# Kernel tuning notes

Measured on AMD Instinct MI355X. Metric: run time of the kernel, lower is better.

The kernel has to match this reference:

```python
import jax, jax.numpy as jnp
import numpy as np
from jax import lax

VOCAB = 50000
EMB = 10
HID = 16


def setup_inputs() -> dict:
    key = jax.random.key(0)
    ks = jax.random.split(key, 8)
    B, T = 4096, 512
    x = jax.random.randint(ks[0], (B, T), 0, VOCAB + 1)
    emb = jax.random.normal(ks[1], (VOCAB + 1, EMB), dtype=jnp.float32)
    emb = emb.at[0].set(0.0)  # padding_idx=0 row is zeros
    s_ih = 1.0 / np.sqrt(HID)
    Wih = jax.random.uniform(ks[2], (4 * HID, EMB), minval=-s_ih, maxval=s_ih, dtype=jnp.float32)
    Whh = jax.random.uniform(ks[3], (4 * HID, HID), minval=-s_ih, maxval=s_ih, dtype=jnp.float32)
    bih = jax.random.uniform(ks[4], (4 * HID,), minval=-s_ih, maxval=s_ih, dtype=jnp.float32)
    bhh = jax.random.uniform(ks[5], (4 * HID,), minval=-s_ih, maxval=s_ih, dtype=jnp.float32)
    Wfc = jax.random.uniform(ks[6], (1, HID), minval=-s_ih, maxval=s_ih, dtype=jnp.float32)
    bfc = jax.random.uniform(ks[7], (1,), minval=-s_ih, maxval=s_ih, dtype=jnp.float32)
    return {"x": x, "emb": emb, "Wih": Wih, "Whh": Whh, "bih": bih, "bhh": bhh, "Wfc": Wfc, "bfc": bfc}


def _lstm_last_h(xe, Wih, Whh, bih, bhh):
    # xe: [B, T, EMB] -> final hidden state [B, HID]. PyTorch gate order: i, f, g, o.
    B = xe.shape[0]
    h0 = jnp.zeros((B, HID), dtype=xe.dtype)
    c0 = jnp.zeros((B, HID), dtype=xe.dtype)
    # Precompute input projections for all timesteps: [T, B, 4H]
    xproj = jnp.einsum('btе,ge->btg'.replace('\u0435', 'e'), xe, Wih) + bih + bhh
    xproj = xproj.transpose(1, 0, 2)

    def step(carry, xp_t):
        h, c = carry
        gates = xp_t + h @ Whh.T  # [B, 4H]
        i, f, g, o = jnp.split(gates, 4, axis=-1)
        i = jax.nn.sigmoid(i)
        f = jax.nn.sigmoid(f)
        g = jnp.tanh(g)
        o = jax.nn.sigmoid(o)
        c = f * c + i * g
        h = o * jnp.tanh(c)
        return (h, c), None

    (h, _), _ = lax.scan(step, (h0, c0), xproj)
    return h


def reference(x, emb, Wih, Whh, bih, bhh, Wfc, bfc):
    xe = emb[x]  # [B, T, EMB] embedding lookup (padding row 0 is zero)
    h = _lstm_last_h(xe, Wih, Whh, bih, bhh)  # [B, HID]
    out = h @ Wfc.T + bfc  # [B, 1]
    return jax.nn.sigmoid(out)
```

## Files before the change

### kernel.cpp

```cpp
#include <hip/hip_runtime.h>

#define T_LEN 512
#define NHID 16
#define NEMB 10
#define VOCAB1 50001
#define IROW 521

typedef float v2f __attribute__((ext_vector_type(2)));

__global__ __launch_bounds__(256) void build_table(
    const float* __restrict__ emb, const float* __restrict__ Wih,
    const float* __restrict__ bih, const float* __restrict__ bhh,
    float* __restrict__ tbl)
{
    const int tid = blockIdx.x * 256 + threadIdx.x;
    if (tid >= VOCAB1 * 16) return;
    const int v = tid >> 4, j = tid & 15;
    float e[NEMB];
    #pragma unroll
    for (int i = 0; i < NEMB; ++i) e[i] = emb[v * NEMB + i];
    float o[4];
    #pragma unroll
    for (int q = 0; q < 4; ++q) {
        const int r = q * 16 + j;
        float a = bih[r] + bhh[r];
        #pragma unroll
        for (int i = 0; i < NEMB; ++i) a += e[i] * Wih[r * NEMB + i];
        o[q] = a;
    }
    ((float4*)tbl)[tid] = make_float4(o[0], o[1], o[2], o[3]);
}

__global__ __launch_bounds__(256) void lstm_dpk_kernel(
    const int*   __restrict__ x,
    const float* __restrict__ tbl,
    const float* __restrict__ Whh,
    const float* __restrict__ Wfc,
    const float* __restrict__ bfc,
    float*       __restrict__ out)
{
    __shared__ int idxs[16][IROW];

    const int tid = threadIdx.x;
    const int j   = tid & 15;
    const int lb  = tid >> 4;
    const int batch = blockIdx.x * 16 + lb;

    #pragma unroll 1
    for (int b = 0; b < 16; ++b) {
        const int* xr = x + (size_t)(blockIdx.x * 16 + b) * T_LEN;
        for (int t = tid; t < IROW; t += 256)
            idxs[b][t] = (t < T_LEN) ? (xr[t] << 4) : 0;
    }
    __syncthreads();

    v2f wp[4][8];
    #pragma unroll
    for (int q = 0; q < 4; ++q) {
        const int row = (q * 16 + j) * NHID;
        #pragma unroll
        for (int s = 0; s < 8; ++s)
            wp[q][s] = (v2f){Whh[row + ((j - 2 * s) & 15)],
                             Whh[row + ((j - 2 * s - 1) & 15)]};
    }

    float h = 0.f, c = 0.f;
    const float NL2E  = -1.44269504088896f;
    const float NL2E2 = -2.88539008177793f;
    const float4* t4 = (const float4*)tbl;

    float4 pf[4];
    int iv[4];
    #pragma unroll
    for (int s = 0; s < 4; ++s) {
        pf[s] = t4[idxs[lb][s] + j];
        iv[s] = idxs[lb][4 + s];
    }

    #pragma unroll 1
    for (int t = 0; t < T_LEN; t += 4) {
        int ivn[4];
        #pragma unroll
        for (int u = 0; u < 4; ++u) ivn[u] = idxs[lb][t + 8 + u];

        #pragma unroll
        for (int u = 0; u < 4; ++u) {
            const float4 tb = pf[u];
            pf[u] = t4[iv[u] + j];

            const int hvi = __builtin_bit_cast(int, h);
            #define ROR(r) __builtin_bit_cast(float, \
                __builtin_amdgcn_update_dpp(0, hvi, 0x120 + (r), 0xF, 0xF, true))
            v2f hrp[8];
            hrp[0] = (v2f){h,       ROR(1)};
            hrp[1] = (v2f){ROR(2),  ROR(3)};
            hrp[2] = (v2f){ROR(4),  ROR(5)};
            hrp[3] = (v2f){ROR(6),  ROR(7)};
            hrp[4] = (v2f){ROR(8),  ROR(9)};
            hrp[5] = (v2f){ROR(10), ROR(11)};
            hrp[6] = (v2f){ROR(12), ROR(13)};
            hrp[7] = (v2f){ROR(14), ROR(15)};
            #undef ROR

            v2f a0 = (v2f){tb.x, 0.f}, b0 = (v2f){0.f, 0.f};
            v2f a1 = (v2f){tb.y, 0.f}, b1 = (v2f){0.f, 0.f};
            v2f a2 = (v2f){tb.z, 0.f}, b2 = (v2f){0.f, 0.f};
            v2f a3 = (v2f){tb.w, 0.f}, b3 = (v2f){0.f, 0.f};
            #pragma unroll
            for (int s = 0; s < 4; ++s) {
                a0 += hrp[s] * wp[0][s];  b0 += hrp[s + 4] * wp[0][s + 4];
                a1 += hrp[s] * wp[1][s];  b1 += hrp[s + 4] * wp[1][s + 4];
                a2 += hrp[s] * wp[2][s];  b2 += hrp[s + 4] * wp[2][s + 4];
                a3 += hrp[s] * wp[3][s];  b3 += hrp[s + 4] * wp[3][s + 4];
            }
            const v2f s0 = a0 + b0, s1 = a1 + b1, s2 = a2 + b2, s3 = a3 + b3;
            const float v0 = s0.x + s0.y, v1 = s1.x + s1.y;
            const float v2 = s2.x + s2.y, v3 = s3.x + s3.y;

            const float ig = __builtin_amdgcn_rcpf(1.f + __builtin_amdgcn_exp2f(v0 * NL2E));
            const float fg = __builtin_amdgcn_rcpf(1.f + __builtin_amdgcn_exp2f(v1 * NL2E));
            const float gg = 2.f * __builtin_amdgcn_rcpf(1.f + __builtin_amdgcn_exp2f(v2 * NL2E2)) - 1.f;
            const float og = __builtin_amdgcn_rcpf(1.f + __builtin_amdgcn_exp2f(v3 * NL2E));

            c = fg * c + ig * gg;
            const float tc = 2.f * __builtin_amdgcn_rcpf(1.f + __builtin_amdgcn_exp2f(c * NL2E2)) - 1.f;
            h = og * tc;
        }

        #pragma unroll
        for (int u = 0; u < 4; ++u) iv[u] = ivn[u];
    }

    float s = h * Wfc[j];
    s += __shfl_xor(s, 1, 64);
    s += __shfl_xor(s, 2, 64);
    s += __shfl_xor(s, 4, 64);
    s += __shfl_xor(s, 8, 64);
    if (j == 0)
        out[batch] = __builtin_amdgcn_rcpf(1.f + __builtin_amdgcn_exp2f((s + bfc[0]) * NL2E));
}

__global__ __launch_bounds__(256) void lstm_fb_kernel(
    const int*   __restrict__ x,
    const float* __restrict__ emb,
    const float* __restrict__ Wih,
    const float* __restrict__ Whh,
    const float* __restrict__ bih,
    const float* __restrict__ bhh,
    const float* __restrict__ Wfc,
    const float* __restrict__ bfc,
    float*       __restrict__ out)
{
    __shared__ int   idx_lds[T_LEN][17];
    __shared__ float hx[16][20];

    const int tid  = threadIdx.x;
    const int lane = tid & 63;
    const int j    = lane & 15;
    const int lb   = tid >> 4;
    const int batch = blockIdx.x * 16 + lb;

    for (int i = tid; i < 16 * T_LEN; i += 256) {
        const int b = i & 15;
        const int t = i >> 4;
        idx_lds[t][b] = x[(blockIdx.x * 16 + b) * T_LEN + t];
    }

    float wih[4][NEMB], bias[4];
    v2f w[4][8];
    #pragma unroll
    for (int q = 0; q < 4; ++q) {
        const int r = j + 16 * q;
        #pragma unroll
        for (int e = 0; e < NEMB; ++e) wih[q][e] = Wih[r * NEMB + e];
        #pragma unroll
        for (int p = 0; p < 8; ++p)
            w[q][p] = (v2f){Whh[r * NHID + 2 * p], Whh[r * NHID + 2 * p + 1]};
        bias[q] = bih[r] + bhh[r];
    }

    __syncthreads();

    v2f h2[8];
    #pragma unroll
    for (int p = 0; p < 8; ++p) h2[p] = (v2f){0.f, 0.f};
    float c = 0.f;

    const float NL2E  = -1.44269504088896f;
    const float NL2E2 = -2.88539008177793f;
    const float4* hp = (const float4*)&hx[lb][0];

    float2 xa, xb, xc, xd, xe2;
    {
        const float2* er = (const float2*)(emb + (long)idx_lds[0][lb] * NEMB);
        xa = er[0]; xb = er[1]; xc = er[2]; xd = er[3]; xe2 = er[4];
    }
    int idx_n = idx_lds[1][lb];

    #pragma unroll 1
    for (int t = 0; t < T_LEN; ++t) {
        const float xv[NEMB] = {xa.x, xa.y, xb.x, xb.y, xc.x, xc.y,
                                xd.x, xd.y, xe2.x, xe2.y};
        if (t + 1 < T_LEN) {
            const float2* er = (const float2*)(emb + (long)idx_n * NEMB);
            xa = er[0]; xb = er[1]; xc = er[2]; xd = er[3]; xe2 = er[4];
        }
        const int idx_nn = (t + 2 < T_LEN) ? idx_lds[t + 2][lb] : 0;

        float v[4];
        #pragma unroll
        for (int q = 0; q < 4; ++q) {
            float a = bias[q];
            #pragma unroll
            for (int e = 0; e < NEMB; ++e) a += xv[e] * wih[q][e];
            v[q] = a;
        }
        v2f a0 = (v2f){v[0], 0.f}, a1 = (v2f){v[1], 0.f};
        v2f a2 = (v2f){v[2], 0.f}, a3 = (v2f){v[3], 0.f};
        #pragma unroll
        for (int p = 0; p < 8; ++p) {
            a0 += h2[p] * w[0][p];
            a1 += h2[p] * w[1][p];
            a2 += h2[p] * w[2][p];
            a3 += h2[p] * w[3][p];
        }
        const float vi = a0.x + a0.y, vf = a1.x + a1.y;
        const float vg = a2.x + a2.y, vo = a3.x + a3.y;

        const float ig = __builtin_amdgcn_rcpf(1.f + __builtin_amdgcn_exp2f(vi * NL2E));
        const float fg = __builtin_amdgcn_rcpf(1.f + __builtin_amdgcn_exp2f(vf * NL2E));
        const float gg = 2.f * __builtin_amdgcn_rcpf(1.f + __builtin_amdgcn_exp2f(vg * NL2E2)) - 1.f;
        const float og = __builtin_amdgcn_rcpf(1.f + __builtin_amdgcn_exp2f(vo * NL2E));

        c = fg * c + ig * gg;
        const float tc = 2.f * __builtin_amdgcn_rcpf(1.f + __builtin_amdgcn_exp2f(c * NL2E2)) - 1.f;
        const float hv = og * tc;

        hx[lb][j] = hv;
        const float4 b0 = hp[0], b1 = hp[1], b2 = hp[2], b3 = hp[3];
        h2[0] = (v2f){b0.x, b0.y}; h2[1] = (v2f){b0.z, b0.w};
        h2[2] = (v2f){b1.x, b1.y}; h2[3] = (v2f){b1.z, b1.w};
        h2[4] = (v2f){b2.x, b2.y}; h2[5] = (v2f){b2.z, b2.w};
        h2[6] = (v2f){b3.x, b3.y}; h2[7] = (v2f){b3.z, b3.w};

        idx_n = idx_nn;
    }

    if (j == 0) {
        float logit = bfc[0];
        #pragma unroll
        for (int p = 0; p < 8; ++p)
            logit += h2[p].x * Wfc[2 * p] + h2[p].y * Wfc[2 * p + 1];
        out[batch] = __builtin_amdgcn_rcpf(1.f + __builtin_amdgcn_exp2f(logit * NL2E));
    }
}

extern "C" void kernel_launch(void* const* d_in, const int* in_sizes, int n_in,
                              void* d_out, int out_size, void* d_ws, size_t ws_size,
                              hipStream_t stream) {
    const int*   x   = (const int*)  d_in[0];
    const float* emb = (const float*)d_in[1];
    const float* Wih = (const float*)d_in[2];
    const float* Whh = (const float*)d_in[3];
    const float* bih = (const float*)d_in[4];
    const float* bhh = (const float*)d_in[5];
    const float* Wfc = (const float*)d_in[6];
    const float* bfc = (const float*)d_in[7];
    float* outp = (float*)d_out;

    const int B = in_sizes[0] / T_LEN;
    const size_t TABLE_BYTES = (size_t)VOCAB1 * 64 * sizeof(float);

    if (ws_size >= TABLE_BYTES) {
        float* tbl = (float*)d_ws;
        build_table<<<(VOCAB1 * 16 + 255) / 256, 256, 0, stream>>>(emb, Wih, bih, bhh, tbl);
        lstm_dpk_kernel<<<B / 16, 256, 0, stream>>>(x, tbl, Whh, Wfc, bfc, outp);
    } else {
        lstm_fb_kernel<<<B / 16, 256, 0, stream>>>(x, emb, Wih, Whh, bih, bhh, Wfc, bfc, outp);
    }
}
```

Before: 164.0 us.

## Split LSTM gate computation across two lane halves per batch row

Each batch row now uses 32 lanes instead of 16. Each half-group computes two of the four gate pre-activations: lanes with hi=0 compute i and f, and lanes with hi=1 compute g and o. The halves then exchange results with a ds_swizzle. The table layout is changed to match, so each lane fetches a float2 rather than a float4. This halves the per-step serial dot-product and transcendental work on the recurrence critical path, but doubles the thread count, halves the rows per block, and adds cross-lane swizzle latency each step.

```diff
diff --git a/kernel.cpp b/kernel.cpp
--- a/kernel.cpp
+++ b/kernel.cpp
@@ -8,7 +8,7 @@
 
 typedef float v2f __attribute__((ext_vector_type(2)));
 
-__global__ __launch_bounds__(256) void build_table(
+__global__ __launch_bounds__(256) void build_table2(
     const float* __restrict__ emb, const float* __restrict__ Wih,
     const float* __restrict__ bih, const float* __restrict__ bhh,
     float* __restrict__ tbl)
@@ -28,10 +28,15 @@
         for (int i = 0; i < NEMB; ++i) a += e[i] * Wih[r * NEMB + i];
         o[q] = a;
     }
-    ((float4*)tbl)[tid] = make_float4(o[0], o[1], o[2], o[3]);
-}
-
-__global__ __launch_bounds__(256) void lstm_dpk_kernel(
+    float2* t2 = (float2*)tbl;
+    t2[v * 32 + j]      = make_float2(o[0], o[1]);
+    t2[v * 32 + 16 + j] = make_float2(o[2], o[3]);
+}
+
+#define ROR_F(hvi, r) __builtin_bit_cast(float, \
+    __builtin_amdgcn_update_dpp(0, hvi, 0x120 + (r), 0xF, 0xF, true))
+
+__global__ __launch_bounds__(256) void lstm_gs_kernel(
     const int*   __restrict__ x,
     const float* __restrict__ tbl,
     const float* __restrict__ Whh,
@@ -39,41 +44,51 @@
     const float* __restrict__ bfc,
     float*       __restrict__ out)
 {
-    __shared__ int idxs[16][IROW];
+    __shared__ int idxs[8][IROW];
 
     const int tid = threadIdx.x;
-    const int j   = tid & 15;
-    const int lb  = tid >> 4;
-    const int batch = blockIdx.x * 16 + lb;
+    const int l   = tid & 63;
+    const int j   = l & 15;
+    const int hi  = (l >> 4) & 1;
+    const int lb  = tid >> 5;
+    const int batch = blockIdx.x * 8 + lb;
 
     #pragma unroll 1
-    for (int b = 0; b < 16; ++b) {
-        const int* xr = x + (size_t)(blockIdx.x * 16 + b) * T_LEN;
+    for (int b = 0; b < 8; ++b) {
+        const int* xr = x + (size_t)(blockIdx.x * 8 + b) * T_LEN;
         for (int t = tid; t < IROW; t += 256)
-            idxs[b][t] = (t < T_LEN) ? (xr[t] << 4) : 0;
+            idxs[b][t] = (t < T_LEN) ? (xr[t] << 5) : 0;
     }
     __syncthreads();
 
-    v2f wp[4][8];
-    #pragma unroll
-    for (int q = 0; q < 4; ++q) {
-        const int row = (q * 16 + j) * NHID;
-        #pragma unroll
-        for (int s = 0; s < 8; ++s)
-            wp[q][s] = (v2f){Whh[row + ((j - 2 * s) & 15)],
-                             Whh[row + ((j - 2 * s - 1) & 15)]};
-    }
-
-    float h = 0.f, c = 0.f;
+    v2f wpA[8], wpB[8];
+    {
+        const int rA = (2 * hi) * 16 + j;
+        const int rB = rA + 16;
+        #pragma unroll
+        for (int s = 0; s < 8; ++s) {
+            const int k0 = (j - 2 * s) & 15, k1 = (j - 2 * s - 1) & 15;
+            wpA[s] = (v2f){Whh[rA * NHID + k0], Whh[rA * NHID + k1]};
+            wpB[s] = (v2f){Whh[rB * NHID + k0], Whh[rB * NHID + k1]};
+        }
+    }
+
     const float NL2E  = -1.44269504088896f;
     const float NL2E2 = -2.88539008177793f;
-    const float4* t4 = (const float4*)tbl;
-
-    float4 pf[4];
+    const bool  hib = (hi != 0);
+    const float sA = hib ? NL2E2 : NL2E;
+    const float mA = hib ? 2.f : 1.f;
+    const float bA = hib ? -1.f : 0.f;
+
+    float h = 0.f, c = 0.f;
+    const float2* t2 = (const float2*)tbl;
+    const int foff = hi * 16 + j;
+
+    float2 pf[4];
     int iv[4];
     #pragma unroll
     for (int s = 0; s < 4; ++s) {
-        pf[s] = t4[idxs[lb][s] + j];
+        pf[s] = t2[idxs[lb][s] + foff];
         iv[s] = idxs[lb][4 + s];
     }
 
@@ -85,46 +100,47 @@
 
         #pragma unroll
         for (int u = 0; u < 4; ++u) {
-            const float4 tb = pf[u];
-            pf[u] = t4[iv[u] + j];
+            const float2 tb = pf[u];
+            pf[u] = t2[iv[u] + foff];
 
             const int hvi = __builtin_bit_cast(int, h);
-            #define ROR(r) __builtin_bit_cast(float, \
-                __builtin_amdgcn_update_dpp(0, hvi, 0x120 + (r), 0xF, 0xF, true))
             v2f hrp[8];
-            hrp[0] = (v2f){h,       ROR(1)};
-            hrp[1] = (v2f){ROR(2),  ROR(3)};
-            hrp[2] = (v2f){ROR(4),  ROR(5)};
-            hrp[3] = (v2f){ROR(6),  ROR(7)};
-            hrp[4] = (v2f){ROR(8),  ROR(9)};
-            hrp[5] = (v2f){ROR(10), ROR(11)};
-            hrp[6] = (v2f){ROR(12), ROR(13)};
-            hrp[7] = (v2f){ROR(14), ROR(15)};
-            #undef ROR
-
-            v2f a0 = (v2f){tb.x, 0.f}, b0 = (v2f){0.f, 0.f};
-            v2f a1 = (v2f){tb.y, 0.f}, b1 = (v2f){0.f, 0.f};
-            v2f a2 = (v2f){tb.z, 0.f}, b2 = (v2f){0.f, 0.f};
-            v2f a3 = (v2f){tb.w, 0.f}, b3 = (v2f){0.f, 0.f};
+            hrp[0] = (v2f){h,             ROR_F(hvi, 1)};
+            hrp[1] = (v2f){ROR_F(hvi, 2),  ROR_F(hvi, 3)};
+            hrp[2] = (v2f){ROR_F(hvi, 4),  ROR_F(hvi, 5)};
+            hrp[3] = (v2f){ROR_F(hvi, 6),  ROR_F(hvi, 7)};
+            hrp[4] = (v2f){ROR_F(hvi, 8),  ROR_F(hvi, 9)};
+            hrp[5] = (v2f){ROR_F(hvi, 10), ROR_F(hvi, 11)};
+            hrp[6] = (v2f){ROR_F(hvi, 12), ROR_F(hvi, 13)};
+            hrp[7] = (v2f){ROR_F(hvi, 14), ROR_F(hvi, 15)};
+
+            v2f aA0 = (v2f){tb.x, 0.f}, aA1 = (v2f){0.f, 0.f};
+            v2f aB0 = (v2f){tb.y, 0.f}, aB1 = (v2f){0.f, 0.f};
             #pragma unroll
             for (int s = 0; s < 4; ++s) {
-                a0 += hrp[s] * wp[0][s];  b0 += hrp[s + 4] * wp[0][s + 4];
-                a1 += hrp[s] * wp[1][s];  b1 += hrp[s + 4] * wp[1][s + 4];
-                a2 += hrp[s] * wp[2][s];  b2 += hrp[s + 4] * wp[2][s + 4];
-                a3 += hrp[s] * wp[3][s];  b3 += hrp[s + 4] * wp[3][s + 4];
+                aA0 += hrp[s] * wpA[s];  aA1 += hrp[s + 4] * wpA[s + 4];
+                aB0 += hrp[s] * wpB[s];  aB1 += hrp[s + 4] * wpB[s + 4];
             }
-            const v2f s0 = a0 + b0, s1 = a1 + b1, s2 = a2 + b2, s3 = a3 + b3;
-            const float v0 = s0.x + s0.y, v1 = s1.x + s1.y;
-            const float v2 = s2.x + s2.y, v3 = s3.x + s3.y;
-
-            const float ig = __builtin_amdgcn_rcpf(1.f + __builtin_amdgcn_exp2f(v0 * NL2E));
-            const float fg = __builtin_amdgcn_rcpf(1.f + __builtin_amdgcn_exp2f(v1 * NL2E));
-            const float gg = 2.f * __builtin_amdgcn_rcpf(1.f + __builtin_amdgcn_exp2f(v2 * NL2E2)) - 1.f;
-            const float og = __builtin_amdgcn_rcpf(1.f + __builtin_amdgcn_exp2f(v3 * NL2E));
-
-            c = fg * c + ig * gg;
+            const v2f sAv = aA0 + aA1, sBv = aB0 + aB1;
+            const float vA = sAv.x + sAv.y;
+            const float vB = sBv.x + sBv.y;
+
+            const float gA = __builtin_amdgcn_rcpf(1.f + __builtin_amdgcn_exp2f(vA * sA)) * mA + bA;
+            const float gB = __builtin_amdgcn_rcpf(1.f + __builtin_amdgcn_exp2f(vB * NL2E));
+
+            const float othA = __builtin_bit_cast(float,
+                __builtin_amdgcn_ds_swizzle(__builtin_bit_cast(int, gA), 0x401F));
+            const float othB = __builtin_bit_cast(float,
+                __builtin_amdgcn_ds_swizzle(__builtin_bit_cast(int, gB), 0x401F));
+
+            const float ii = hib ? othA : gA;
+            const float ff = hib ? othB : gB;
+            const float gg = hib ? gA : othA;
+            const float oo = hib ? gB : othB;
+
+            c = ff * c + ii * gg;
             const float tc = 2.f * __builtin_amdgcn_rcpf(1.f + __builtin_amdgcn_exp2f(c * NL2E2)) - 1.f;
-            h = og * tc;
+            h = oo * tc;
         }
 
         #pragma unroll
@@ -136,7 +152,7 @@
     s += __shfl_xor(s, 2, 64);
     s += __shfl_xor(s, 4, 64);
     s += __shfl_xor(s, 8, 64);
-    if (j == 0)
+    if ((l & 31) == 0)
         out[batch] = __builtin_amdgcn_rcpf(1.f + __builtin_amdgcn_exp2f((s + bfc[0]) * NL2E));
 }
 
@@ -273,8 +289,8 @@
 
     if (ws_size >= TABLE_BYTES) {
         float* tbl = (float*)d_ws;
-        build_table<<<(VOCAB1 * 16 + 255) / 256, 256, 0, stream>>>(emb, Wih, bih, bhh, tbl);
-        lstm_dpk_kernel<<<B / 16, 256, 0, stream>>>(x, tbl, Whh, Wfc, bfc, outp);
+        build_table2<<<(VOCAB1 * 16 + 255) / 256, 256, 0, stream>>>(emb, Wih, bih, bhh, tbl);
+        lstm_gs_kernel<<<B / 8, 256, 0, stream>>>(x, tbl, Whh, Wfc, bfc, outp);
     } else {
         lstm_fb_kernel<<<B / 16, 256, 0, stream>>>(x, emb, Wih, Whh, bih, bhh, Wfc, bfc, outp);
     }
```

Measured after the change: 185.2 us. 12.9% more time.
